# Optimization experiments

Measured on AMD Instinct MI355X. Metric: run time of the kernel, lower is better.

Reference implementation:

```python
import jax, jax.numpy as jnp
import numpy as np

B, S, D, E, H, F, L, C = 32768, 5, 512, 256, 4, 2048, 2, 5  # batch, sensors, input_dim, embed_dim, heads, ffn, layers, classes
DH = E // H
EPS = 1e-5


def layer_norm(x, g, b):
    m = jnp.mean(x, axis=-1, keepdims=True)
    v = jnp.mean((x - m) ** 2, axis=-1, keepdims=True)
    return (x - m) * jax.lax.rsqrt(v + EPS) * g + b


def setup_inputs() -> dict:
    key = jax.random.key(0)
    ks = jax.random.split(key, 24)
    n = lambda k, shape: (jax.random.normal(k, shape, dtype=jnp.float32) * 0.02)
    return {
        "x": jax.random.normal(ks[0], (B, S, D), dtype=jnp.float32),
        "sensor_types": jax.random.randint(ks[1], (B, S), 0, 2, dtype=jnp.int32),
        "gps_w": n(ks[2], (E, D)), "gps_b": jnp.zeros((E,), jnp.float32),
        "ang_w": n(ks[3], (E, D)), "ang_b": jnp.zeros((E,), jnp.float32),
        "qkv_w": n(ks[4], (L, 3 * E, E)), "qkv_b": jnp.zeros((L, 3 * E), jnp.float32),
        "attn_ow": n(ks[5], (L, E, E)), "attn_ob": jnp.zeros((L, E), jnp.float32),
        "ln1_g": jnp.ones((L, E), jnp.float32), "ln1_b": jnp.zeros((L, E), jnp.float32),
        "ff1_w": n(ks[6], (L, F, E)), "ff1_b": jnp.zeros((L, F), jnp.float32),
        "ff2_w": n(ks[7], (L, E, F)), "ff2_b": jnp.zeros((L, E), jnp.float32),
        "ln2_g": jnp.ones((L, E), jnp.float32), "ln2_b": jnp.zeros((L, E), jnp.float32),
        "fc1_w": n(ks[8], (128, S * E)), "fc1_b": jnp.zeros((128,), jnp.float32),
        "fc2_w": n(ks[9], (64, 128)), "fc2_b": jnp.zeros((64,), jnp.float32),
        "out_w": n(ks[10], (C, 64)), "out_b": jnp.zeros((C,), jnp.float32),
    }


def reference(x, sensor_types, gps_w, gps_b, ang_w, ang_b, qkv_w, qkv_b,
              attn_ow, attn_ob, ln1_g, ln1_b, ff1_w, ff1_b, ff2_w, ff2_b,
              ln2_g, ln2_b, fc1_w, fc1_b, fc2_w, fc2_b, out_w, out_b):
    # Dual-expert routing: compute both branches, blend by mask (same math as masked scatter)
    is_gps = (sensor_types == 0)[..., None]  # [B,S,1]
    g = jax.nn.relu(jnp.einsum('bsd,ed->bse', x, gps_w) + gps_b)
    a = jax.nn.relu(jnp.einsum('bsd,ed->bse', x, ang_w) + ang_b)
    h = jnp.where(is_gps, g, a)  # [B,S,E]

    # TransformerEncoder (post-LN, ReLU FFN, dropout inactive at eval)
    for l in range(L):
        qkv = jnp.einsum('bse,fe->bsf', h, qkv_w[l]) + qkv_b[l]  # [B,S,3E]
        q, k, v = jnp.split(qkv, 3, axis=-1)
        q = q.reshape(B, S, H, DH); k = k.reshape(B, S, H, DH); v = v.reshape(B, S, H, DH)
        scores = jnp.einsum('bqhd,bkhd->bhqk', q, k) / jnp.sqrt(jnp.float32(DH))
        attn = jax.nn.softmax(scores, axis=-1)
        o = jnp.einsum('bhqk,bkhd->bqhd', attn, v).reshape(B, S, E)
        o = o @ attn_ow[l].T + attn_ob[l]
        h = layer_norm(h + o, ln1_g[l], ln1_b[l])
        ff = jax.nn.relu(h @ ff1_w[l].T + ff1_b[l]) @ ff2_w[l].T + ff2_b[l]
        h = layer_norm(h + ff, ln2_g[l], ln2_b[l])

    z = h.reshape(B, S * E)
    z = z @ fc1_w.T + fc1_b
    z = z @ fc2_w.T + fc2_b
    return z @ out_w.T + out_b
```

## Files before the change

kernel.cpp:

```cpp
#include <hip/hip_runtime.h>


#define N_TOK 163840
#define NBATCH 32768

typedef __attribute__((ext_vector_type(8))) short bfrag;
typedef __attribute__((ext_vector_type(4))) float f32x4;

__device__ __forceinline__ float bf2f(ushort u) {
  return __builtin_bit_cast(float, (uint)u << 16);
}
__device__ __forceinline__ ushort f2bf(float f) {
  uint u = __builtin_bit_cast(uint, f);
  return (ushort)((u + 0x7FFFu + ((u >> 16) & 1u)) >> 16);
}

__global__ __launch_bounds__(256) void cvt_kernel(const float* __restrict__ in,
                                                  ushort* __restrict__ out, int n4) {
  int i = blockIdx.x * 256 + threadIdx.x;
  if (i >= n4) return;
  float4 v = ((const float4*)in)[i];
  ushort4 o;
  o.x = f2bf(v.x); o.y = f2bf(v.y); o.z = f2bf(v.z); o.w = f2bf(v.w);
  ((ushort4*)out)[i] = o;
}

enum { EPI_F32 = 0, EPI_F32_RELU = 1, EPI_BF16 = 2, EPI_BF16_RELU = 3 };

template <int EPI>
__global__ __launch_bounds__(256) void gemm_bt(const ushort* __restrict__ A,
                                               const ushort* __restrict__ W,
                                               const float* __restrict__ bias,
                                               void* __restrict__ outp,
                                               int M, int K, int O) {
  __shared__ ushort As[128][40];
  __shared__ ushort Bs[128][40];
  const int tid = threadIdx.x;
  const int wave = tid >> 6, lane = tid & 63;
  const int bm = blockIdx.y, bn = blockIdx.x;
  const int wm = (wave & 1) << 6, wn = (wave >> 1) << 6;
  const int srow = tid >> 2;
  const int scol = (tid & 3) << 3;

  const ushort* Abase = A + (size_t)bm * 128 * K + (size_t)srow * K + scol;
  const ushort* Wbase = W + (size_t)bn * 128 * K + (size_t)srow * K + scol;

  f32x4 acc[4][4];
#pragma unroll
  for (int i = 0; i < 4; i++)
#pragma unroll
    for (int j = 0; j < 4; j++) acc[i][j] = {0.f, 0.f, 0.f, 0.f};

  const int fr = lane & 15;
  const int fkb = (lane >> 4) << 3;

  for (int k0 = 0; k0 < K; k0 += 32) {
    __syncthreads();
    uint4 a0 = *(const uint4*)(Abase + k0);
    uint4 a1 = *(const uint4*)(Abase + k0 + (size_t)64 * K);
    uint4 b0 = *(const uint4*)(Wbase + k0);
    uint4 b1 = *(const uint4*)(Wbase + k0 + (size_t)64 * K);
    *(uint4*)&As[srow][scol]      = a0;
    *(uint4*)&As[srow + 64][scol] = a1;
    *(uint4*)&Bs[srow][scol]      = b0;
    *(uint4*)&Bs[srow + 64][scol] = b1;
    __syncthreads();
    bfrag af[4], bf_[4];
#pragma unroll
    for (int i = 0; i < 4; i++) af[i] = *(const bfrag*)&As[wm + i * 16 + fr][fkb];
#pragma unroll
    for (int j = 0; j < 4; j++) bf_[j] = *(const bfrag*)&Bs[wn + j * 16 + fr][fkb];
#pragma unroll
    for (int i = 0; i < 4; i++)
#pragma unroll
      for (int j = 0; j < 4; j++)
        acc[i][j] = __builtin_amdgcn_mfma_f32_16x16x32_bf16(af[i], bf_[j], acc[i][j], 0, 0, 0);
  }

  const int cr = (lane >> 4) << 2;
  const int cc = lane & 15;
#pragma unroll
  for (int j = 0; j < 4; j++) {
    const int col = bn * 128 + wn + j * 16 + cc;
    const float bv = bias[col];
#pragma unroll
    for (int i = 0; i < 4; i++) {
      const size_t rbase = (size_t)(bm * 128 + wm + i * 16 + cr) * O + col;
#pragma unroll
      for (int r = 0; r < 4; r++) {
        float v = acc[i][j][r] + bv;
        if (EPI == EPI_F32_RELU || EPI == EPI_BF16_RELU) v = fmaxf(v, 0.f);
        if (EPI == EPI_F32 || EPI == EPI_F32_RELU)
          ((float*)outp)[rbase + (size_t)r * O] = v;
        else
          ((ushort*)outp)[rbase + (size_t)r * O] = f2bf(v);
      }
    }
  }
}

__global__ __launch_bounds__(256) void select_kernel(const float* __restrict__ gbuf,
                                                     float* __restrict__ h32,
                                                     ushort* __restrict__ h16,
                                                     const int* __restrict__ stype) {
  const size_t i4 = (size_t)blockIdx.x * 256 + threadIdx.x;
  const int sel = stype[i4 >> 6];
  float4 gv = *(const float4*)&gbuf[i4 * 4];
  float4 av = *(const float4*)&h32[i4 * 4];
  float4 h = (sel == 0) ? gv : av;
  *(float4*)&h32[i4 * 4] = h;
  ushort4 hb = {f2bf(h.x), f2bf(h.y), f2bf(h.z), f2bf(h.w)};
  *(ushort4*)&h16[i4 * 4] = hb;
}

__global__ __launch_bounds__(256) void attn_kernel(const ushort* __restrict__ qkv,
                                                   ushort* __restrict__ o16) {
  __shared__ ushort s_qkv[8 * 5 * 768];
  __shared__ float s_att[8 * 4 * 25];
  const int tid = threadIdx.x;
  const size_t gbase = (size_t)blockIdx.x * (8 * 5 * 768);
#pragma unroll
  for (int t = 0; t < 15; t++) {
    int i = tid + t * 256;
    *(uint4*)&s_qkv[i * 8] = *(const uint4*)(qkv + gbase + (size_t)i * 8);
  }
  __syncthreads();
  for (int idx = tid; idx < 800; idx += 256) {
    int b = idx / 100, r = idx - b * 100;
    int h = r / 25, ij = r - h * 25;
    int i = ij / 5, j = ij - i * 5;
    const ushort* qp = &s_qkv[(b * 5 + i) * 768 + h * 64];
    const ushort* kp = &s_qkv[(b * 5 + j) * 768 + 256 + h * 64];
    float s = 0.f;
#pragma unroll
    for (int d = 0; d < 64; d += 2) {
      uint qw = *(const uint*)&qp[d];
      uint kw = *(const uint*)&kp[d];
      s += bf2f((ushort)(qw & 0xffffu)) * bf2f((ushort)(kw & 0xffffu));
      s += bf2f((ushort)(qw >> 16)) * bf2f((ushort)(kw >> 16));
    }
    s_att[idx] = s * 0.125f;
  }
  __syncthreads();
  if (tid < 160) {
    float* sp = &s_att[tid * 5];
    float m = fmaxf(fmaxf(fmaxf(sp[0], sp[1]), fmaxf(sp[2], sp[3])), sp[4]);
    float e0 = __expf(sp[0] - m), e1 = __expf(sp[1] - m), e2 = __expf(sp[2] - m);
    float e3 = __expf(sp[3] - m), e4 = __expf(sp[4] - m);
    float inv = 1.f / (e0 + e1 + e2 + e3 + e4);
    sp[0] = e0 * inv; sp[1] = e1 * inv; sp[2] = e2 * inv; sp[3] = e3 * inv; sp[4] = e4 * inv;
  }
  __syncthreads();
  const size_t obase = (size_t)blockIdx.x * (8 * 5 * 256);
#pragma unroll
  for (int t = 0; t < 40; t++) {
    int idx = t * 256 + tid;
    int d = idx & 63;
    int rest = idx >> 6;
    int h = rest & 3; rest >>= 2;
    int i = rest % 5, b = rest / 5;
    const float* ap = &s_att[(b * 4 + h) * 25 + i * 5];
    const ushort* vp = &s_qkv[(b * 5) * 768 + 512 + h * 64 + d];
    float o = 0.f;
#pragma unroll
    for (int j = 0; j < 5; j++) o += ap[j] * bf2f(vp[j * 768]);
    o16[obase + (size_t)((b * 5 + i) * 256 + h * 64 + d)] = f2bf(o);
  }
}

__global__ __launch_bounds__(256) void ln_res_kernel(const float* __restrict__ t,
                                                     float* __restrict__ h32,
                                                     ushort* __restrict__ h16,
                                                     const float* __restrict__ g,
                                                     const float* __restrict__ b) {
  const int wave = threadIdx.x >> 6, lane = threadIdx.x & 63;
  const size_t row = (size_t)blockIdx.x * 4 + wave;
  const size_t off = row * 256 + lane * 4;
  float4 tv = *(const float4*)&t[off];
  float4 hv = *(const float4*)&h32[off];
  float4 u = {tv.x + hv.x, tv.y + hv.y, tv.z + hv.z, tv.w + hv.w};
  float s = u.x + u.y + u.z + u.w;
  float sq = u.x * u.x + u.y * u.y + u.z * u.z + u.w * u.w;
#pragma unroll
  for (int o = 32; o > 0; o >>= 1) { s += __shfl_xor(s, o); sq += __shfl_xor(sq, o); }
  float mean = s * 0.00390625f;
  float var = sq * 0.00390625f - mean * mean;
  float rstd = rsqrtf(var + 1e-5f);
  float4 gv = *(const float4*)&g[lane * 4];
  float4 bv = *(const float4*)&b[lane * 4];
  float4 y = {(u.x - mean) * rstd * gv.x + bv.x, (u.y - mean) * rstd * gv.y + bv.y,
              (u.z - mean) * rstd * gv.z + bv.z, (u.w - mean) * rstd * gv.w + bv.w};
  *(float4*)&h32[off] = y;
  ushort4 hb = {f2bf(y.x), f2bf(y.y), f2bf(y.z), f2bf(y.w)};
  *(ushort4*)&h16[off] = hb;
}

__global__ __launch_bounds__(256) void head2_kernel(const float* __restrict__ z1,
                                                    const float* __restrict__ fc2w,
                                                    const float* __restrict__ fc2b,
                                                    const float* __restrict__ outw,
                                                    const float* __restrict__ outb,
                                                    float* __restrict__ out) {
  __shared__ float s_z2[4][64];
  const int wave = threadIdx.x >> 6, lane = threadIdx.x & 63;
  const int b = blockIdx.x * 4 + wave;
  const float* z = z1 + (size_t)b * 128;
  float acc = fc2b[lane];
#pragma unroll 8
  for (int k = 0; k < 128; k++) acc += z[k] * fc2w[lane * 128 + k];
  s_z2[wave][lane] = acc;
  __syncthreads();
  if (lane < 5) {
    const float* zz = s_z2[wave];
    float o = outb[lane];
#pragma unroll 8
    for (int k = 0; k < 64; k++) o += zz[k] * outw[lane * 64 + k];
    out[(size_t)b * 5 + lane] = o;
  }
}

extern "C" void kernel_launch(void* const* d_in, const int* in_sizes, int n_in,
                              void* d_out, int out_size, void* d_ws, size_t ws_size,
                              hipStream_t stream) {
  const float* x       = (const float*)d_in[0];
  const int*   stype   = (const int*)d_in[1];
  const float* gps_w   = (const float*)d_in[2];
  const float* gps_b   = (const float*)d_in[3];
  const float* ang_w   = (const float*)d_in[4];
  const float* ang_b   = (const float*)d_in[5];
  const float* qkv_w   = (const float*)d_in[6];
  const float* qkv_b   = (const float*)d_in[7];
  const float* attn_ow = (const float*)d_in[8];
  const float* attn_ob = (const float*)d_in[9];
  const float* ln1_g   = (const float*)d_in[10];
  const float* ln1_b   = (const float*)d_in[11];
  const float* ff1_w   = (const float*)d_in[12];
  const float* ff1_b   = (const float*)d_in[13];
  const float* ff2_w   = (const float*)d_in[14];
  const float* ff2_b   = (const float*)d_in[15];
  const float* fc1_w   = (const float*)d_in[16 + 2];
  const float* fc1_b   = (const float*)d_in[19];
  const float* fc2_w   = (const float*)d_in[20];
  const float* fc2_b   = (const float*)d_in[21];
  const float* out_w   = (const float*)d_in[22];
  const float* out_b   = (const float*)d_in[23];
  const float* ln2_g   = (const float*)d_in[16];
  const float* ln2_b   = (const float*)d_in[17];

  char* ws = (char*)d_ws;
  const size_t NEED = 763363328ull;
  if (ws_size < NEED) return;

  ushort* w_gps  = (ushort*)ws;
  ushort* w_ang  = w_gps + 131072;
  ushort* w_qkv  = w_ang + 131072;
  ushort* w_attn = w_qkv + 393216;
  ushort* w_ff1  = w_attn + 131072;
  ushort* w_ff2  = w_ff1 + 1048576;
  ushort* w_fc1  = w_ff2 + 1048576;

  ushort* R16 = (ushort*)(ws + (size_t)(8u << 20));
  ushort* h16 = (ushort*)(ws + 8388608ull + 251658240ull);
  float*  h32 = (float*)(ws + 8388608ull + 251658240ull + 83886080ull);
  float*  t32 = (float*)(ws + 8388608ull + 251658240ull + 83886080ull + 167772160ull);
  ushort* o16 = (ushort*)(ws + 8388608ull + 251658240ull + 83886080ull + 335544320ull);

  auto cvt = [&](const float* src, ushort* dst, int n4) {
    cvt_kernel<<<(n4 + 255) / 256, 256, 0, stream>>>(src, dst, n4);
  };
  cvt(gps_w, w_gps, 32768);
  cvt(ang_w, w_ang, 32768);
  cvt(qkv_w, w_qkv, 98304);
  cvt(attn_ow, w_attn, 32768);
  cvt(ff1_w, w_ff1, 262144);
  cvt(ff2_w, w_ff2, 262144);
  cvt(fc1_w, w_fc1, 40960);
  cvt(x, R16, 20971520);

  gemm_bt<EPI_F32_RELU><<<dim3(2, 1280), 256, 0, stream>>>(R16, w_gps, gps_b, t32, N_TOK, 512, 256);
  gemm_bt<EPI_F32_RELU><<<dim3(2, 1280), 256, 0, stream>>>(R16, w_ang, ang_b, h32, N_TOK, 512, 256);
  select_kernel<<<40960, 256, 0, stream>>>(t32, h32, h16, stype);

  for (int l = 0; l < 2; l++) {
    gemm_bt<EPI_BF16><<<dim3(6, 1280), 256, 0, stream>>>(h16, w_qkv + l * 196608, qkv_b + l * 768,
                                                         R16, N_TOK, 256, 768);
    attn_kernel<<<4096, 256, 0, stream>>>(R16, o16);
    gemm_bt<EPI_F32><<<dim3(2, 1280), 256, 0, stream>>>(o16, w_attn + l * 65536, attn_ob + l * 256,
                                                        t32, N_TOK, 256, 256);
    ln_res_kernel<<<40960, 256, 0, stream>>>(t32, h32, h16, ln1_g + l * 256, ln1_b + l * 256);
    for (int c = 0; c < 4; c++) {
      gemm_bt<EPI_BF16_RELU><<<dim3(16, 320), 256, 0, stream>>>(
          h16 + (size_t)c * 40960 * 256, w_ff1 + l * 524288, ff1_b + l * 2048, R16, 40960, 256, 2048);
      gemm_bt<EPI_F32><<<dim3(2, 320), 256, 0, stream>>>(
          R16, w_ff2 + l * 524288, ff2_b + l * 256, t32 + (size_t)c * 40960 * 256, 40960, 2048, 256);
    }
    ln_res_kernel<<<40960, 256, 0, stream>>>(t32, h32, h16, ln2_g + l * 256, ln2_b + l * 256);
  }

  gemm_bt<EPI_F32><<<dim3(1, 256), 256, 0, stream>>>(h16, w_fc1, fc1_b, t32, NBATCH, 1280, 128);
  head2_kernel<<<8192, 256, 0, stream>>>(t32, fc2_w, fc2_b, out_w, out_b, (float*)d_out);
}
```

Baseline: 3.495 ms.

## Fuse residual LayerNorm and expert select into GEMM epilogues, use direct global-to-LDS loads

```diff
diff --git a/kernel.cpp b/kernel.cpp
--- a/kernel.cpp
+++ b/kernel.cpp
@@ -13,6 +13,12 @@
 __device__ __forceinline__ ushort f2bf(float f) {
   uint u = __builtin_bit_cast(uint, f);
   return (ushort)((u + 0x7FFFu + ((u >> 16) & 1u)) >> 16);
+}
+
+__device__ __forceinline__ void gl2lds16(const ushort* g, ushort* l) {
+  __builtin_amdgcn_global_load_lds(
+      (const __attribute__((address_space(1))) unsigned int*)g,
+      (__attribute__((address_space(3))) unsigned int*)l, 16, 0, 0);
 }
 
 __global__ __launch_bounds__(256) void cvt_kernel(const float* __restrict__ in,
@@ -25,25 +31,30 @@
   ((ushort4*)out)[i] = o;
 }
 
-enum { EPI_F32 = 0, EPI_F32_RELU = 1, EPI_BF16 = 2, EPI_BF16_RELU = 3 };
+enum { EPI_F32 = 0, EPI_F32_RELU = 1, EPI_BF16 = 2, EPI_BF16_RELU = 3, EPI_SELECT = 4 };
 
 template <int EPI>
 __global__ __launch_bounds__(256) void gemm_bt(const ushort* __restrict__ A,
                                                const ushort* __restrict__ W,
                                                const float* __restrict__ bias,
                                                void* __restrict__ outp,
-                                               int M, int K, int O) {
-  __shared__ ushort As[128][40];
-  __shared__ ushort Bs[128][40];
+                                               int M, int K, int O,
+                                               const float* __restrict__ gbuf,
+                                               const int* __restrict__ stype,
+                                               ushort* __restrict__ h16out) {
+  __shared__ ushort As[128][32];
+  __shared__ ushort Bs[128][32];
   const int tid = threadIdx.x;
   const int wave = tid >> 6, lane = tid & 63;
   const int bm = blockIdx.y, bn = blockIdx.x;
   const int wm = (wave & 1) << 6, wn = (wave >> 1) << 6;
-  const int srow = tid >> 2;
-  const int scol = (tid & 3) << 3;
-
-  const ushort* Abase = A + (size_t)bm * 128 * K + (size_t)srow * K + scol;
-  const ushort* Wbase = W + (size_t)bn * 128 * K + (size_t)srow * K + scol;
+
+  const int srow = wave * 16 + (lane >> 2);
+  const int scol = (lane & 3) << 3;
+  const ushort* Ag = A + (size_t)(bm * 128 + srow) * K + scol;
+  const ushort* Wg = W + (size_t)(bn * 128 + srow) * K + scol;
+  ushort* AsP = &As[srow][scol];
+  ushort* BsP = &Bs[srow][scol];
 
   f32x4 acc[4][4];
 #pragma unroll
@@ -56,14 +67,10 @@
 
   for (int k0 = 0; k0 < K; k0 += 32) {
     __syncthreads();
-    uint4 a0 = *(const uint4*)(Abase + k0);
-    uint4 a1 = *(const uint4*)(Abase + k0 + (size_t)64 * K);
-    uint4 b0 = *(const uint4*)(Wbase + k0);
-    uint4 b1 = *(const uint4*)(Wbase + k0 + (size_t)64 * K);
-    *(uint4*)&As[srow][scol]      = a0;
-    *(uint4*)&As[srow + 64][scol] = a1;
-    *(uint4*)&Bs[srow][scol]      = b0;
-    *(uint4*)&Bs[srow + 64][scol] = b1;
+    gl2lds16(Ag + k0, AsP);
+    gl2lds16(Ag + k0 + (size_t)64 * K, AsP + 64 * 32);
+    gl2lds16(Wg + k0, BsP);
+    gl2lds16(Wg + k0 + (size_t)64 * K, BsP + 64 * 32);
     __syncthreads();
     bfrag af[4], bf_[4];
 #pragma unroll
@@ -85,32 +92,124 @@
     const float bv = bias[col];
 #pragma unroll
     for (int i = 0; i < 4; i++) {
-      const size_t rbase = (size_t)(bm * 128 + wm + i * 16 + cr) * O + col;
+      const int row = bm * 128 + wm + i * 16 + cr;
 #pragma unroll
       for (int r = 0; r < 4; r++) {
         float v = acc[i][j][r] + bv;
-        if (EPI == EPI_F32_RELU || EPI == EPI_BF16_RELU) v = fmaxf(v, 0.f);
-        if (EPI == EPI_F32 || EPI == EPI_F32_RELU)
-          ((float*)outp)[rbase + (size_t)r * O] = v;
-        else
-          ((ushort*)outp)[rbase + (size_t)r * O] = f2bf(v);
+        const size_t idx = (size_t)(row + r) * O + col;
+        if (EPI != EPI_F32 && EPI != EPI_BF16) v = fmaxf(v, 0.f);
+        if (EPI == EPI_SELECT) {
+          if (stype[row + r] == 0) v = gbuf[idx];
+          ((float*)outp)[idx] = v;
+          h16out[idx] = f2bf(v);
+        } else if (EPI == EPI_F32 || EPI == EPI_F32_RELU) {
+          ((float*)outp)[idx] = v;
+        } else {
+          ((ushort*)outp)[idx] = f2bf(v);
+        }
       }
     }
   }
 }
 
-__global__ __launch_bounds__(256) void select_kernel(const float* __restrict__ gbuf,
-                                                     float* __restrict__ h32,
-                                                     ushort* __restrict__ h16,
-                                                     const int* __restrict__ stype) {
-  const size_t i4 = (size_t)blockIdx.x * 256 + threadIdx.x;
-  const int sel = stype[i4 >> 6];
-  float4 gv = *(const float4*)&gbuf[i4 * 4];
-  float4 av = *(const float4*)&h32[i4 * 4];
-  float4 h = (sel == 0) ? gv : av;
-  *(float4*)&h32[i4 * 4] = h;
-  ushort4 hb = {f2bf(h.x), f2bf(h.y), f2bf(h.z), f2bf(h.w)};
-  *(ushort4*)&h16[i4 * 4] = hb;
+__global__ __launch_bounds__(512) void gemm_lnres(const ushort* __restrict__ A,
+                                                  const ushort* __restrict__ W,
+                                                  const float* __restrict__ bias,
+                                                  float* __restrict__ h32,
+                                                  ushort* __restrict__ h16,
+                                                  const float* __restrict__ g,
+                                                  const float* __restrict__ b,
+                                                  int K) {
+  __shared__ ushort As[128][32];
+  __shared__ ushort Bs[256][32];
+  __shared__ float2 s_part[128][4];
+  __shared__ float2 s_mr[128];
+  const int tid = threadIdx.x;
+  const int wave = tid >> 6, lane = tid & 63;
+  const int bm = blockIdx.x;
+  const int wm = (wave & 1) << 6, wn = (wave >> 1) << 6;
+
+  const int srow = wave * 16 + (lane >> 2);
+  const int scol = (lane & 3) << 3;
+  const ushort* Ag = A + (size_t)(bm * 128 + srow) * K + scol;
+  const ushort* Wg = W + (size_t)srow * K + scol;
+  ushort* AsP = &As[srow][scol];
+  ushort* BsP = &Bs[srow][scol];
+
+  f32x4 acc[4][4];
+#pragma unroll
+  for (int i = 0; i < 4; i++)
+#pragma unroll
+    for (int j = 0; j < 4; j++) acc[i][j] = {0.f, 0.f, 0.f, 0.f};
+
+  const int fr = lane & 15;
+  const int fkb = (lane >> 4) << 3;
+
+  for (int k0 = 0; k0 < K; k0 += 32) {
+    __syncthreads();
+    gl2lds16(Ag + k0, AsP);
+    gl2lds16(Wg + k0, BsP);
+    gl2lds16(Wg + k0 + (size_t)128 * K, BsP + 128 * 32);
+    __syncthreads();
+    bfrag af[4], bf_[4];
+#pragma unroll
+    for (int i = 0; i < 4; i++) af[i] = *(const bfrag*)&As[wm + i * 16 + fr][fkb];
+#pragma unroll
+    for (int j = 0; j < 4; j++) bf_[j] = *(const bfrag*)&Bs[wn + j * 16 + fr][fkb];
+#pragma unroll
+    for (int i = 0; i < 4; i++)
+#pragma unroll
+      for (int j = 0; j < 4; j++)
+        acc[i][j] = __builtin_amdgcn_mfma_f32_16x16x32_bf16(af[i], bf_[j], acc[i][j], 0, 0, 0);
+  }
+
+  const int cr = (lane >> 4) << 2;
+  const int cc = lane & 15;
+#pragma unroll
+  for (int i = 0; i < 4; i++) {
+#pragma unroll
+    for (int r = 0; r < 4; r++) {
+      const int row = wm + i * 16 + cr + r;
+      const size_t grow = (size_t)(bm * 128 + row) * 256;
+      float s = 0.f, sq = 0.f;
+#pragma unroll
+      for (int j = 0; j < 4; j++) {
+        const int col = wn + j * 16 + cc;
+        float u = acc[i][j][r] + bias[col] + h32[grow + col];
+        acc[i][j][r] = u;
+        s += u; sq += u * u;
+      }
+#pragma unroll
+      for (int o = 1; o < 16; o <<= 1) { s += __shfl_xor(s, o); sq += __shfl_xor(sq, o); }
+      if ((lane & 15) == 0) s_part[row][wave >> 1] = {s, sq};
+    }
+  }
+  __syncthreads();
+  if (tid < 128) {
+    float2 p0 = s_part[tid][0], p1 = s_part[tid][1], p2 = s_part[tid][2], p3 = s_part[tid][3];
+    float S = p0.x + p1.x + p2.x + p3.x;
+    float SQ = p0.y + p1.y + p2.y + p3.y;
+    float mean = S * 0.00390625f;
+    float var = SQ * 0.00390625f - mean * mean;
+    s_mr[tid] = {mean, rsqrtf(var + 1e-5f)};
+  }
+  __syncthreads();
+#pragma unroll
+  for (int i = 0; i < 4; i++) {
+#pragma unroll
+    for (int r = 0; r < 4; r++) {
+      const int row = wm + i * 16 + cr + r;
+      const float2 mr = s_mr[row];
+      const size_t grow = (size_t)(bm * 128 + row) * 256;
+#pragma unroll
+      for (int j = 0; j < 4; j++) {
+        const int col = wn + j * 16 + cc;
+        float y = (acc[i][j][r] - mr.x) * mr.y * g[col] + b[col];
+        h32[grow + col] = y;
+        h16[grow + col] = f2bf(y);
+      }
+    }
+  }
 }
 
 __global__ __launch_bounds__(256) void attn_kernel(const ushort* __restrict__ qkv,
@@ -166,33 +265,6 @@
     for (int j = 0; j < 5; j++) o += ap[j] * bf2f(vp[j * 768]);
     o16[obase + (size_t)((b * 5 + i) * 256 + h * 64 + d)] = f2bf(o);
   }
-}
-
-__global__ __launch_bounds__(256) void ln_res_kernel(const float* __restrict__ t,
-                                                     float* __restrict__ h32,
-                                                     ushort* __restrict__ h16,
-                                                     const float* __restrict__ g,
-                                                     const float* __restrict__ b) {
-  const int wave = threadIdx.x >> 6, lane = threadIdx.x & 63;
-  const size_t row = (size_t)blockIdx.x * 4 + wave;
-  const size_t off = row * 256 + lane * 4;
-  float4 tv = *(const float4*)&t[off];
-  float4 hv = *(const float4*)&h32[off];
-  float4 u = {tv.x + hv.x, tv.y + hv.y, tv.z + hv.z, tv.w + hv.w};
-  float s = u.x + u.y + u.z + u.w;
-  float sq = u.x * u.x + u.y * u.y + u.z * u.z + u.w * u.w;
-#pragma unroll
-  for (int o = 32; o > 0; o >>= 1) { s += __shfl_xor(s, o); sq += __shfl_xor(sq, o); }
-  float mean = s * 0.00390625f;
-  float var = sq * 0.00390625f - mean * mean;
-  float rstd = rsqrtf(var + 1e-5f);
-  float4 gv = *(const float4*)&g[lane * 4];
-  float4 bv = *(const float4*)&b[lane * 4];
-  float4 y = {(u.x - mean) * rstd * gv.x + bv.x, (u.y - mean) * rstd * gv.y + bv.y,
-              (u.z - mean) * rstd * gv.z + bv.z, (u.w - mean) * rstd * gv.w + bv.w};
-  *(float4*)&h32[off] = y;
-  ushort4 hb = {f2bf(y.x), f2bf(y.y), f2bf(y.z), f2bf(y.w)};
-  *(ushort4*)&h16[off] = hb;
 }
 
 __global__ __launch_bounds__(256) void head2_kernel(const float* __restrict__ z1,
@@ -238,14 +310,14 @@
   const float* ff1_b   = (const float*)d_in[13];
   const float* ff2_w   = (const float*)d_in[14];
   const float* ff2_b   = (const float*)d_in[15];
-  const float* fc1_w   = (const float*)d_in[16 + 2];
+  const float* ln2_g   = (const float*)d_in[16];
+  const float* ln2_b   = (const float*)d_in[17];
+  const float* fc1_w   = (const float*)d_in[18];
   const float* fc1_b   = (const float*)d_in[19];
   const float* fc2_w   = (const float*)d_in[20];
   const float* fc2_b   = (const float*)d_in[21];
   const float* out_w   = (const float*)d_in[22];
   const float* out_b   = (const float*)d_in[23];
-  const float* ln2_g   = (const float*)d_in[16];
-  const float* ln2_b   = (const float*)d_in[17];
 
   char* ws = (char*)d_ws;
   const size_t NEED = 763363328ull;
@@ -277,26 +349,30 @@
   cvt(fc1_w, w_fc1, 40960);
   cvt(x, R16, 20971520);
 
-  gemm_bt<EPI_F32_RELU><<<dim3(2, 1280), 256, 0, stream>>>(R16, w_gps, gps_b, t32, N_TOK, 512, 256);
-  gemm_bt<EPI_F32_RELU><<<dim3(2, 1280), 256, 0, stream>>>(R16, w_ang, ang_b, h32, N_TOK, 512, 256);
-  select_kernel<<<40960, 256, 0, stream>>>(t32, h32, h16, stype);
+  gemm_bt<EPI_F32_RELU><<<dim3(2, 1280), 256, 0, stream>>>(
+      R16, w_gps, gps_b, t32, N_TOK, 512, 256, nullptr, nullptr, nullptr);
+  gemm_bt<EPI_SELECT><<<dim3(2, 1280), 256, 0, stream>>>(
+      R16, w_ang, ang_b, h32, N_TOK, 512, 256, t32, stype, h16);
 
   for (int l = 0; l < 2; l++) {
-    gemm_bt<EPI_BF16><<<dim3(6, 1280), 256, 0, stream>>>(h16, w_qkv + l * 196608, qkv_b + l * 768,
-                                                         R16, N_TOK, 256, 768);
+    gemm_bt<EPI_BF16><<<dim3(6, 1280), 256, 0, stream>>>(
+        h16, w_qkv + l * 196608, qkv_b + l * 768, R16, N_TOK, 256, 768,
+        nullptr, nullptr, nullptr);
     attn_kernel<<<4096, 256, 0, stream>>>(R16, o16);
-    gemm_bt<EPI_F32><<<dim3(2, 1280), 256, 0, stream>>>(o16, w_attn + l * 65536, attn_ob + l * 256,
-                                                        t32, N_TOK, 256, 256);
-    ln_res_kernel<<<40960, 256, 0, stream>>>(t32, h32, h16, ln1_g + l * 256, ln1_b + l * 256);
+    gemm_lnres<<<1280, 512, 0, stream>>>(o16, w_attn + l * 65536, attn_ob + l * 256,
+                                         h32, h16, ln1_g + l * 256, ln1_b + l * 256, 256);
     for (int c = 0; c < 4; c++) {
       gemm_bt<EPI_BF16_RELU><<<dim3(16, 320), 256, 0, stream>>>(
-          h16 + (size_t)c * 40960 * 256, w_ff1 + l * 524288, ff1_b + l * 2048, R16, 40960, 256, 2048);
-      gemm_bt<EPI_F32><<<dim3(2, 320), 256, 0, stream>>>(
-          R16, w_ff2 + l * 524288, ff2_b + l * 256, t32 + (size_t)c * 40960 * 256, 40960, 2048, 256);
-    }
-    ln_res_kernel<<<40960, 256, 0, stream>>>(t32, h32, h16, ln2_g + l * 256, ln2_b + l * 256);
-  }
-
-  gemm_bt<EPI_F32><<<dim3(1, 256), 256, 0, stream>>>(h16, w_fc1, fc1_b, t32, NBATCH, 1280, 128);
+          h16 + (size_t)c * 40960 * 256, w_ff1 + l * 524288, ff1_b + l * 2048,
+          R16, 40960, 256, 2048, nullptr, nullptr, nullptr);
+      gemm_lnres<<<320, 512, 0, stream>>>(R16, w_ff2 + l * 524288, ff2_b + l * 256,
+                                          h32 + (size_t)c * 40960 * 256,
+                                          h16 + (size_t)c * 40960 * 256,
+                                          ln2_g + l * 256, ln2_b + l * 256, 2048);
+    }
+  }
+
+  gemm_bt<EPI_F32><<<dim3(1, 256), 256, 0, stream>>>(
+      h16, w_fc1, fc1_b, t32, NBATCH, 1280, 128, nullptr, nullptr, nullptr);
   head2_kernel<<<8192, 256, 0, stream>>>(t32, fc2_w, fc2_b, out_w, out_b, (float*)d_out);
 }
```

Measured after the change: 3.970 ms. +13.6%, slower.
